# Kernel tuning notes

Measured on AMD Instinct MI355X. Metric: run time of the kernel, lower is better.

Reference implementation:

```python
import jax, jax.numpy as jnp
import numpy as np

B, N, DIM = 16, 1024, 768


def setup_inputs() -> dict:
    key = jax.random.key(0)
    ks = jax.random.split(key, 8)
    x = jax.random.normal(ks[0], (B, N, DIM), dtype=jnp.float32)
    y = jax.random.normal(ks[1], (B, N, DIM), dtype=jnp.float32)
    coords = jax.random.normal(ks[2], (N, N, 6), dtype=jnp.float32)
    # orthogonal init for U (as in torch init.orthogonal_)
    a = jax.random.normal(ks[3], (DIM, DIM), dtype=jnp.float32)
    q, r = jnp.linalg.qr(a)
    U = q * jnp.sign(jnp.diagonal(r))[None, :]
    S1 = jnp.ones((DIM,), dtype=jnp.float32)
    S2 = jnp.ones((DIM,), dtype=jnp.float32)
    gating = jnp.asarray(1.0, dtype=jnp.float32)
    temp = jnp.asarray(0.1, dtype=jnp.float32)
    pos_emb = jnp.zeros((N, 6, 1), dtype=jnp.float32)
    return {"x": x, "y": y, "coords": coords, "U": U, "S1": S1, "S2": S2,
            "gating": gating, "temp": temp, "pos_emb": pos_emb}


def reference(x, y, coords, U, S1, S2, gating, temp, pos_emb):
    dim = x.shape[-1]
    scale = dim ** (-0.5)
    # spectral decomposition: x @ U^T @ diag(S^2) @ U
    xu = x @ U.T                                   # [B,N,d]
    x1 = (xu * jnp.square(S1)) @ U                 # [B,N,d]
    x2 = (xu * jnp.square(S2)) @ U                 # [B,N,d]
    xs = jnp.stack([x1, x2], axis=1)               # [B,2,N,d]
    patch_score = jax.nn.softmax(
        jnp.einsum('bknd,bmd->bknm', xs, y) * scale, axis=-1)  # [B,2,N,M]
    pos = jnp.squeeze(coords @ pos_emb, -1)        # [N,M]
    pos_score = jax.nn.softmax(pos, axis=-1)[None, None]        # [1,1,N,M]
    g = jax.nn.sigmoid(gating)
    attn = (1.0 - g) * patch_score + g * pos_score  # [B,2,N,M]
    # entropy-routed gating
    entropy = jnp.sum(-attn * jnp.log(attn + 1e-8), axis=-1)    # [B,2,N]
    hmap = 2.0 - 2.0 * jax.nn.sigmoid(temp * jnp.transpose(entropy, (0, 2, 1)))  # [B,N,2]
    fgbg = hmap[..., 0] >= hmap[..., 1]
    route = jax.lax.stop_gradient(
        jnp.stack([fgbg, ~fgbg], axis=-1).astype(hmap.dtype))   # [B,N,2]
    heat_map = jnp.sum(hmap * route, axis=-1, keepdims=True)    # [B,N,1]
    attn_c = jnp.sum(attn * jnp.transpose(route, (0, 2, 1))[..., None], axis=1)  # [B,N,M]
    out = attn_c @ y                               # [B,N,d]
    return (out, heat_map)
```

## Files before the change

### kernel.cpp

```cpp
#include <hip/hip_runtime.h>
#include <hip/hip_bf16.h>

#define DEV __device__ __forceinline__

typedef unsigned short u16;
typedef short short8 __attribute__((ext_vector_type(8)));
typedef u16 u16x4 __attribute__((ext_vector_type(4)));
typedef float f32x16 __attribute__((ext_vector_type(16)));

static const int BB = 16;
static const int NN = 1024;
static const int DD = 768;

DEV u16 f2bf(float f) {
    unsigned u = __builtin_bit_cast(unsigned, f);
    unsigned r = u + 0x7fffu + ((u >> 16) & 1u);
    return (u16)(r >> 16);
}
DEV float h2f(u16 u) { return (float)__builtin_bit_cast(_Float16, u); }
DEV u16 f2h(float f) { return __builtin_bit_cast(u16, (_Float16)f); }

DEV void gl_lds16(const void* g, void* l) {
    __builtin_amdgcn_global_load_lds(
        (const __attribute__((address_space(1))) unsigned int*)g,
        (__attribute__((address_space(3))) unsigned int*)l, 16, 0, 0);
}

DEV void fence_bar() {
    asm volatile("" ::: "memory");
    __builtin_amdgcn_s_barrier();
    asm volatile("" ::: "memory");
}
DEV void wait_vm4() { asm volatile("s_waitcnt vmcnt(4)" ::: "memory"); }

template<int OM>
__global__ __launch_bounds__(256, 3) void gemm128(
    const u16* __restrict__ Ag, const u16* __restrict__ Bg, void* __restrict__ Cg,
    int K, int N, int zmod,
    long sA0, long sA1, long sB0, long sB1, long sC0, long sC1,
    float scale)
{
    __shared__ u16 As[128 * 64];
    __shared__ u16 Bs[128 * 64];

    int z = blockIdx.z;
    const u16* A = Ag + (long)(z % zmod) * sA0 + (long)(z / zmod) * sA1;
    const u16* B = Bg + (long)(z % zmod) * sB0 + (long)(z / zmod) * sB1;
    u16*   Cu = (u16*)Cg   + (long)(z % zmod) * sC0 + (long)(z / zmod) * sC1;
    float* Cf = (float*)Cg + (long)(z % zmod) * sC0 + (long)(z / zmod) * sC1;

    int tid  = threadIdx.x;
    int lane = tid & 63, wave = tid >> 6;
    int wm = wave & 1, wn = wave >> 1;
    int ln31 = lane & 31, khalf = lane >> 5;

    long m0 = (long)blockIdx.x * 128;
    long n0 = (long)blockIdx.y * 128;

    long aOfs[4], bOfs[4];
    u16 *lA[4], *lB[4];
#pragma unroll
    for (int i = 0; i < 4; i++) {
        int p = tid + i * 256;
        int row = p >> 3, qs = p & 7;
        int q = qs ^ (row & 7);
        aOfs[i] = (m0 + row) * (long)K + q * 8;
        bOfs[i] = (n0 + row) * (long)K + q * 8;
        lA[i] = As + p * 8;
        lB[i] = Bs + p * 8;
    }

    int aoff[2][4], boff[2][4];
#pragma unroll
    for (int t = 0; t < 2; t++) {
        int ra = wm * 64 + t * 32 + ln31;
        int rb = wn * 64 + t * 32 + ln31;
#pragma unroll
        for (int h = 0; h < 4; h++) {
            aoff[t][h] = ra * 64 + (((h * 2 + khalf) ^ (ra & 7)) * 8);
            boff[t][h] = rb * 64 + (((h * 2 + khalf) ^ (rb & 7)) * 8);
        }
    }

    f32x16 acc[2][2] = {};

    for (int k0 = 0; k0 < K; k0 += 64) {
#pragma unroll
        for (int i = 0; i < 4; i++) gl_lds16(A + aOfs[i] + k0, lA[i]);
#pragma unroll
        for (int i = 0; i < 4; i++) gl_lds16(B + bOfs[i] + k0, lB[i]);
        __syncthreads();

#pragma unroll
        for (int h = 0; h < 4; h++) {
            short8 af[2], bfr[2];
#pragma unroll
            for (int t = 0; t < 2; t++) af[t]  = *(const short8*)(As + aoff[t][h]);
#pragma unroll
            for (int t = 0; t < 2; t++) bfr[t] = *(const short8*)(Bs + boff[t][h]);
#pragma unroll
            for (int ti = 0; ti < 2; ti++)
#pragma unroll
                for (int tj = 0; tj < 2; tj++)
                    acc[ti][tj] = __builtin_amdgcn_mfma_f32_32x32x16_bf16(
                        af[ti], bfr[tj], acc[ti][tj], 0, 0, 0);
        }
        __syncthreads();
    }

    long crow = m0 + wm * 64 + 4 * khalf;
    long ccol = n0 + wn * 64 + ln31;
#pragma unroll
    for (int ti = 0; ti < 2; ti++)
#pragma unroll
        for (int tj = 0; tj < 2; tj++)
#pragma unroll
            for (int r = 0; r < 16; r++) {
                long row = crow + ti * 32 + (r & 3) + 8 * (r >> 2);
                long col = ccol + tj * 32;
                float v = acc[ti][tj][r] * scale;
                long idx = row * (long)N + col;
                if constexpr (OM == 0)      Cu[idx] = f2bf(v);
                else if constexpr (OM == 1) Cu[idx] = f2h(v);
                else                        Cf[idx] = v;
            }
}

template<int OM>
__global__ __launch_bounds__(512, 2) void gemm256(
    const u16* __restrict__ Ag, const u16* __restrict__ Bg, void* __restrict__ Cg,
    int K, int N, int zmod,
    long sA0, long sA1, long sB0, long sB1, long sC0, long sC1,
    float scale)
{
    __shared__ u16 lds[2][4][8192];

    int z = blockIdx.z;
    const u16* A = Ag + (long)(z % zmod) * sA0 + (long)(z / zmod) * sA1;
    const u16* B = Bg + (long)(z % zmod) * sB0 + (long)(z / zmod) * sB1;
    u16*   Cu = (u16*)Cg   + (long)(z % zmod) * sC0 + (long)(z / zmod) * sC1;
    float* Cf = (float*)Cg + (long)(z % zmod) * sC0 + (long)(z / zmod) * sC1;

    int tid  = threadIdx.x;
    int lane = tid & 63, wave = tid >> 6;
    int wm = wave >> 2, wn = wave & 3;
    int ln31 = lane & 31, khalf = lane >> 5;

    long m0 = (long)blockIdx.x * 256;
    long n0 = (long)blockIdx.y * 256;
    const u16* Apan = A + m0 * (long)K;
    const u16* Bpan = B + n0 * (long)K;

    long stA[2];
#pragma unroll
    for (int r = 0; r < 2; r++) {
        int p = tid + r * 512;
        int row = p >> 2, c = (p & 3) ^ ((row >> 1) & 3);
        stA[r] = (long)row * K + c * 8;
    }

    int aoffs[4][2], boffs[2][2];
#pragma unroll
    for (int m = 0; m < 4; m++) {
        int rr = wm * 128 + m * 32 + ln31;
#pragma unroll
        for (int sl = 0; sl < 2; sl++)
            aoffs[m][sl] = rr * 32 + (((sl * 2 + khalf) ^ ((rr >> 1) & 3)) * 8);
    }
#pragma unroll
    for (int n = 0; n < 2; n++) {
        int cc = wn * 64 + n * 32 + ln31;
#pragma unroll
        for (int sl = 0; sl < 2; sl++)
            boffs[n][sl] = cc * 32 + (((sl * 2 + khalf) ^ ((cc >> 1) & 3)) * 8);
    }

    f32x16 acc[4][2] = {};

    int nkt = K >> 6;
    int niter = nkt >> 1;

#define STG(PAN, BUF, HSEL, KT, KH) do {                                   \
    const u16* _s0 = (PAN) + stA[0] + (long)(KT) * 64 + (KH) * 32;         \
    const u16* _s1 = (PAN) + stA[1] + (long)(KT) * 64 + (KH) * 32;         \
    u16* _d = &lds[BUF][HSEL][0] + tid * 8;                                \
    gl_lds16(_s0, _d);                                                     \
    gl_lds16(_s1, _d + 4096);                                              \
} while (0)

#define PH(BUF, S, DOSTG, GUARD) do {                                      \
    short8 av[4], bv[2];                                                   \
    _Pragma("unroll")                                                      \
    for (int m = 0; m < 4; m++)                                            \
        av[m] = *(const short8*)(&lds[BUF][(S) >> 1][aoffs[m][(S) & 1]]);  \
    _Pragma("unroll")                                                      \
    for (int n = 0; n < 2; n++)                                            \
        bv[n] = *(const short8*)(&lds[BUF][2 + ((S) >> 1)][boffs[n][(S) & 1]]); \
    DOSTG;                                                                 \
    if (GUARD) wait_vm4();                                                 \
    fence_bar();                                                           \
    __builtin_amdgcn_s_setprio(1);                                         \
    _Pragma("unroll")                                                      \
    for (int m = 0; m < 4; m++)                                            \
        _Pragma("unroll")                                                  \
        for (int n = 0; n < 2; n++)                                        \
            acc[m][n] = __builtin_amdgcn_mfma_f32_32x32x16_bf16(           \
                av[m], bv[n], acc[m][n], 0, 0, 0);                         \
    __builtin_amdgcn_s_setprio(0);                                         \
    fence_bar();                                                           \
} while (0)

    STG(Apan, 0, 0, 0, 0);
    STG(Bpan, 0, 2, 0, 0);
    STG(Apan, 0, 1, 0, 1);
    STG(Bpan, 0, 3, 0, 1);
    STG(Apan, 1, 0, 1, 0);
    STG(Bpan, 1, 2, 1, 0);
    wait_vm4();
    fence_bar();

    for (int it = 0; it < niter; ++it) {
        int t1 = 2 * it + 1;
        int t2 = 2 * it + 2; int t2c = t2 < nkt ? t2 : nkt - 1;
        int t3 = 2 * it + 3; int t3c = t3 < nkt ? t3 : nkt - 1;
        PH(0, 0, STG(Apan, 1, 1, t1,  1), false);
        PH(0, 1, STG(Bpan, 1, 3, t1,  1), false);
        PH(0, 2, STG(Apan, 0, 0, t2c, 0), false);
        PH(0, 3, STG(Bpan, 0, 2, t2c, 0), true);
        PH(1, 0, STG(Apan, 0, 1, t2c, 1), false);
        PH(1, 1, STG(Bpan, 0, 3, t2c, 1), false);
        PH(1, 2, STG(Apan, 1, 0, t3c, 0), false);
        PH(1, 3, STG(Bpan, 1, 2, t3c, 0), true);
    }
#undef PH
#undef STG

    long crow = m0 + wm * 128 + 4 * khalf;
    long ccol = n0 + wn * 64 + ln31;
#pragma unroll
    for (int m = 0; m < 4; m++)
#pragma unroll
        for (int n = 0; n < 2; n++)
#pragma unroll
            for (int r = 0; r < 16; r++) {
                long row = crow + m * 32 + (r & 3) + 8 * (r >> 2);
                long col = ccol + n * 32;
                float v = acc[m][n][r] * scale;
                long idx = row * (long)N + col;
                if constexpr (OM == 0)      Cu[idx] = f2bf(v);
                else if constexpr (OM == 1) Cu[idx] = f2h(v);
                else                        Cf[idx] = v;
            }
}

DEV float wave_red_max(float v) {
#pragma unroll
    for (int o = 32; o; o >>= 1) v = fmaxf(v, __shfl_xor(v, o));
    return v;
}
DEV float wave_red_sum(float v) {
#pragma unroll
    for (int o = 32; o; o >>= 1) v += __shfl_xor(v, o);
    return v;
}
DEV float block_red_max(float v, float* sh) {
    v = wave_red_max(v);
    if ((threadIdx.x & 63) == 0) sh[threadIdx.x >> 6] = v;
    __syncthreads();
    v = fmaxf(fmaxf(sh[0], sh[1]), fmaxf(sh[2], sh[3]));
    __syncthreads();
    return v;
}
DEV float block_red_sum(float v, float* sh) {
    v = wave_red_sum(v);
    if ((threadIdx.x & 63) == 0) sh[threadIdx.x >> 6] = v;
    __syncthreads();
    v = (sh[0] + sh[1]) + (sh[2] + sh[3]);
    __syncthreads();
    return v;
}

__global__ __launch_bounds__(256) void k_prep_all(
    const float* __restrict__ x, const float* __restrict__ y,
    const float* __restrict__ coords, const float* __restrict__ U,
    const float* __restrict__ S1, const float* __restrict__ S2,
    const float* __restrict__ pe,
    u16* __restrict__ xb, u16* __restrict__ yb, u16* __restrict__ yT,
    u16* __restrict__ UTb, u16* __restrict__ VT1, u16* __restrict__ VT2,
    float* __restrict__ P)
{
    __shared__ float shmem[32 * 33];
    int bid = blockIdx.x, tid = threadIdx.x;

    if (bid < 12288) {
        float (*tile)[33] = (float(*)[33])shmem;
        int b = bid / 768, rem = bid % 768;
        int d0 = (rem % 24) * 32, m0 = (rem / 24) * 32;
        int r = tid >> 3, c4 = (tid & 7) * 4;
        const float* ybase = y + (long)b * NN * DD;
        float4 v = *(const float4*)(ybase + (long)(m0 + r) * DD + d0 + c4);
        u16x4 w4;
        w4[0] = f2bf(v.x); w4[1] = f2bf(v.y); w4[2] = f2bf(v.z); w4[3] = f2bf(v.w);
        *(u16x4*)(yb + (long)b * NN * DD + (long)(m0 + r) * DD + d0 + c4) = w4;
        tile[r][c4 + 0] = v.x; tile[r][c4 + 1] = v.y;
        tile[r][c4 + 2] = v.z; tile[r][c4 + 3] = v.w;
        __syncthreads();
        int d = tid >> 3, mq = (tid & 7) * 4;
        u16x4 o;
        o[0] = f2bf(tile[mq + 0][d]); o[1] = f2bf(tile[mq + 1][d]);
        o[2] = f2bf(tile[mq + 2][d]); o[3] = f2bf(tile[mq + 3][d]);
        *(u16x4*)(yT + (long)b * DD * NN + (long)(d0 + d) * NN + m0 + mq) = o;
        return;
    }
    bid -= 12288;

    if (bid < 6144) {
        long base = ((long)bid * 256 + tid) * 8;
        float4 f0 = *(const float4*)(x + base);
        float4 f1 = *(const float4*)(x + base + 4);
        short8 w;
        w[0] = (short)f2bf(f0.x); w[1] = (short)f2bf(f0.y);
        w[2] = (short)f2bf(f0.z); w[3] = (short)f2bf(f0.w);
        w[4] = (short)f2bf(f1.x); w[5] = (short)f2bf(f1.y);
        w[6] = (short)f2bf(f1.z); w[7] = (short)f2bf(f1.w);
        *(short8*)(xb + base) = w;
        return;
    }
    bid -= 6144;

    if (bid < 1024) {
        int n = bid, t = tid;
        float p6[6];
#pragma unroll
        for (int c = 0; c < 6; c++) p6[c] = pe[n * 6 + c];
        float v[4];
#pragma unroll
        for (int i = 0; i < 4; i++) {
            const float* cp = coords + ((long)n * NN + t * 4 + i) * 6;
            v[i] = p6[0]*cp[0] + p6[1]*cp[1] + p6[2]*cp[2]
                 + p6[3]*cp[3] + p6[4]*cp[4] + p6[5]*cp[5];
        }
        float mx = block_red_max(fmaxf(fmaxf(v[0], v[1]), fmaxf(v[2], v[3])), shmem);
        float e[4], s = 0.f;
#pragma unroll
        for (int i = 0; i < 4; i++) { e[i] = expf(v[i] - mx); s += e[i]; }
        float Z = block_red_sum(s, shmem);
        float inv = 1.f / Z;
        float4 o; o.x = e[0]*inv; o.y = e[1]*inv; o.z = e[2]*inv; o.w = e[3]*inv;
        *(float4*)(P + ((long)n << 10) + t * 4) = o;
        return;
    }
    bid -= 1024;

    {
        float (*tile)[33] = (float(*)[33])shmem;
        int i0 = (bid % 24) * 32, j0 = (bid / 24) * 32;
        int tx = tid & 31, ty = tid >> 5;
#pragma unroll
        for (int r = 0; r < 32; r += 8) {
            int i = i0 + ty + r, j = j0 + tx;
            tile[ty + r][tx] = U[(long)i * DD + j];
        }
        __syncthreads();
        float s1v = S1[i0 + tx];
        float s2v = S2[i0 + tx];
        s1v *= s1v; s2v *= s2v;
#pragma unroll
        for (int r = 0; r < 32; r += 8) {
            int j = j0 + ty + r, i = i0 + tx;
            float v = tile[tx][ty + r];
            UTb[(long)j * DD + i] = f2bf(v);
            VT1[(long)j * DD + i] = f2bf(s1v * v);
            VT2[(long)j * DD + i] = f2bf(s2v * v);
        }
    }
}

__global__ __launch_bounds__(64) void k_route(
    u16* __restrict__ S, const float* __restrict__ P,
    const float* __restrict__ gating, const float* __restrict__ temp,
    float* __restrict__ heat)
{
    int bn = blockIdx.x;
    int b = bn >> 10, n = bn & 1023, t = threadIdx.x;
    u16* s1p = S + ((long)(b * 2) << 20) + ((long)n << 10);
    u16* s2p = s1p + (1L << 20);
    const float* pp = P + ((long)n << 10);

    short8 r1a = *(const short8*)(s1p + t * 8);
    short8 r1b = *(const short8*)(s1p + 512 + t * 8);
    short8 r2a = *(const short8*)(s2p + t * 8);
    short8 r2b = *(const short8*)(s2p + 512 + t * 8);
    float4 pv0 = *(const float4*)(pp + t * 8);
    float4 pv1 = *(const float4*)(pp + t * 8 + 4);
    float4 pv2 = *(const float4*)(pp + 512 + t * 8);
    float4 pv3 = *(const float4*)(pp + 512 + t * 8 + 4);

    float s1[16], s2[16], p8[16];
#pragma unroll
    for (int i = 0; i < 8; i++) {
        s1[i]     = h2f((u16)r1a[i]);
        s1[i + 8] = h2f((u16)r1b[i]);
        s2[i]     = h2f((u16)r2a[i]);
        s2[i + 8] = h2f((u16)r2b[i]);
    }
    p8[0]=pv0.x;  p8[1]=pv0.y;  p8[2]=pv0.z;  p8[3]=pv0.w;
    p8[4]=pv1.x;  p8[5]=pv1.y;  p8[6]=pv1.z;  p8[7]=pv1.w;
    p8[8]=pv2.x;  p8[9]=pv2.y;  p8[10]=pv2.z; p8[11]=pv2.w;
    p8[12]=pv3.x; p8[13]=pv3.y; p8[14]=pv3.z; p8[15]=pv3.w;

    float m1 = s1[0], m2 = s2[0];
#pragma unroll
    for (int i = 1; i < 16; i++) { m1 = fmaxf(m1, s1[i]); m2 = fmaxf(m2, s2[i]); }
    float mx1 = wave_red_max(m1);
    float mx2 = wave_red_max(m2);

    float e1[16], e2[16], z1 = 0.f, z2 = 0.f;
#pragma unroll
    for (int i = 0; i < 16; i++) {
        e1[i] = expf(s1[i] - mx1); z1 += e1[i];
        e2[i] = expf(s2[i] - mx2); z2 += e2[i];
    }
    float Z1 = wave_red_sum(z1);
    float Z2 = wave_red_sum(z2);

    float g = 1.f / (1.f + expf(-gating[0]));
    float c1 = (1.f - g) / Z1, c2 = (1.f - g) / Z2;

    float a1[16], a2[16], hh1 = 0.f, hh2 = 0.f;
#pragma unroll
    for (int i = 0; i < 16; i++) {
        a1[i] = e1[i] * c1 + g * p8[i];
        a2[i] = e2[i] * c2 + g * p8[i];
        hh1 -= a1[i] * logf(a1[i] + 1e-8f);
        hh2 -= a2[i] * logf(a2[i] + 1e-8f);
    }
    float H1 = wave_red_sum(hh1);
    float H2 = wave_red_sum(hh2);

    float tv = temp[0];
    float hm0 = 2.f - 2.f / (1.f + expf(-tv * H1));
    float hm1 = 2.f - 2.f / (1.f + expf(-tv * H2));
    int ks = (hm0 >= hm1) ? 0 : 1;
    if (t == 0) heat[bn] = ks ? hm1 : hm0;

    short8 w0, w1;
#pragma unroll
    for (int i = 0; i < 8; i++) {
        w0[i] = (short)f2bf(ks ? a2[i] : a1[i]);
        w1[i] = (short)f2bf(ks ? a2[i + 8] : a1[i + 8]);
    }
    *(short8*)(s1p + t * 8) = w0;
    *(short8*)(s1p + 512 + t * 8) = w1;
}

extern "C" void kernel_launch(void* const* d_in, const int* in_sizes, int n_in,
                              void* d_out, int out_size, void* d_ws, size_t ws_size,
                              hipStream_t stream)
{
    (void)in_sizes; (void)n_in; (void)out_size; (void)ws_size;
    const float* x      = (const float*)d_in[0];
    const float* y      = (const float*)d_in[1];
    const float* coords = (const float*)d_in[2];
    const float* U      = (const float*)d_in[3];
    const float* S1     = (const float*)d_in[4];
    const float* S2     = (const float*)d_in[5];
    const float* gating = (const float*)d_in[6];
    const float* temp   = (const float*)d_in[7];
    const float* pose   = (const float*)d_in[8];

    float* out  = (float*)d_out;
    float* heat = out + (long)BB * NN * DD;

    char* w = (char*)d_ws;
    u16* UTb = (u16*)w;  w += (long)DD * DD * 2;
    u16* VT  = (u16*)w;  w += (long)2 * DD * DD * 2;
    u16* W2  = (u16*)w;  w += (long)2 * DD * DD * 2;
    u16* x12 = (u16*)w;  w += (long)2 * BB * NN * DD * 2;
    u16* yb  = (u16*)w;  w += (long)BB * NN * DD * 2;
    u16* yT  = (u16*)w;  w += (long)BB * DD * NN * 2;
    u16* S   = (u16*)w;  w += (long)BB * 2 * NN * NN * 2;
    float* P = (float*)w;

    u16* xb = S;

    const long MBN = (long)BB * NN * DD;
    const long BND = (long)NN * DD;
    const long SPL = (long)NN * NN;
    const long DSQ = (long)DD * DD;

    k_prep_all<<<dim3(20032), dim3(256), 0, stream>>>(
        x, y, coords, U, S1, S2, pose, xb, yb, yT, UTb, VT, VT + DSQ, P);

    gemm128<0><<<dim3(DD / 128, DD / 128, 2), dim3(256), 0, stream>>>(
        UTb, VT, W2, DD, DD, 2,
        0L, 0L, DSQ, 0L, DSQ, 0L, 1.0f);

    gemm256<0><<<dim3(BB * NN / 256, DD / 256, 2), dim3(512), 0, stream>>>(
        xb, W2, x12, DD, DD, 2,
        0L, 0L, DSQ, 0L, MBN, 0L, 1.0f);

    gemm256<1><<<dim3(NN / 256, NN / 256, BB * 2), dim3(512), 0, stream>>>(
        x12, yb, S, DD, NN, 2,
        MBN, BND, 0L, BND, SPL, 2 * SPL, 0.036084391824351615f);

    k_route<<<dim3(BB * NN), dim3(64), 0, stream>>>(S, P, gating, temp, heat);

    gemm256<2><<<dim3(NN / 256, DD / 256, BB), dim3(512), 0, stream>>>(
        S, yT, out, NN, DD, 1,
        0L, 2 * SPL, 0L, BND, 0L, BND, 1.0f);
}
```

Baseline: 362.5 us.

## Swizzle GEMM workgroup order, split score GEMM, pack route rows, use fast math

Adds an optional workgroup-index swizzle to the 256-tile GEMM that interleaves blocks across eight groups, meant to change which tiles run concurrently and improve cache locality. The score GEMM is split into two launches over half the batch each. The route kernel now handles two rows per 128-thread block, and several exp/log calls are replaced with the fast __expf/__logf intrinsics. The fast intrinsics trade accuracy, and the extra launch adds overhead.

Result: faster. 354.7 us (-2.2%).

```diff
diff --git a/kernel.cpp b/kernel.cpp
--- a/kernel.cpp
+++ b/kernel.cpp
@@ -131,11 +131,21 @@
     const u16* __restrict__ Ag, const u16* __restrict__ Bg, void* __restrict__ Cg,
     int K, int N, int zmod,
     long sA0, long sA1, long sB0, long sB1, long sC0, long sC1,
-    float scale)
+    float scale, int swz)
 {
     __shared__ u16 lds[2][4][8192];
 
-    int z = blockIdx.z;
+    int bx = blockIdx.x, by = blockIdx.y, bz = blockIdx.z;
+    if (swz) {
+        int gx = gridDim.x, gy = gridDim.y;
+        int nwg = gx * gy * gridDim.z;
+        int lin = bx + gx * (by + gy * bz);
+        int sw = (lin & 7) * (nwg >> 3) + (lin >> 3);
+        bx = sw % gx; int t = sw / gx;
+        by = t % gy;  bz = t / gy;
+    }
+
+    int z = bz;
     const u16* A = Ag + (long)(z % zmod) * sA0 + (long)(z / zmod) * sA1;
     const u16* B = Bg + (long)(z % zmod) * sB0 + (long)(z / zmod) * sB1;
     u16*   Cu = (u16*)Cg   + (long)(z % zmod) * sC0 + (long)(z / zmod) * sC1;
@@ -146,8 +156,8 @@
     int wm = wave >> 2, wn = wave & 3;
     int ln31 = lane & 31, khalf = lane >> 5;
 
-    long m0 = (long)blockIdx.x * 256;
-    long n0 = (long)blockIdx.y * 256;
+    long m0 = (long)bx * 256;
+    long n0 = (long)by * 256;
     const u16* Apan = A + m0 * (long)K;
     const u16* Bpan = B + n0 * (long)K;
 
@@ -343,7 +353,7 @@
         float mx = block_red_max(fmaxf(fmaxf(v[0], v[1]), fmaxf(v[2], v[3])), shmem);
         float e[4], s = 0.f;
 #pragma unroll
-        for (int i = 0; i < 4; i++) { e[i] = expf(v[i] - mx); s += e[i]; }
+        for (int i = 0; i < 4; i++) { e[i] = __expf(v[i] - mx); s += e[i]; }
         float Z = block_red_sum(s, shmem);
         float inv = 1.f / Z;
         float4 o; o.x = e[0]*inv; o.y = e[1]*inv; o.z = e[2]*inv; o.w = e[3]*inv;
@@ -376,13 +386,14 @@
     }
 }
 
-__global__ __launch_bounds__(64) void k_route(
+__global__ __launch_bounds__(128) void k_route(
     u16* __restrict__ S, const float* __restrict__ P,
     const float* __restrict__ gating, const float* __restrict__ temp,
     float* __restrict__ heat)
 {
-    int bn = blockIdx.x;
-    int b = bn >> 10, n = bn & 1023, t = threadIdx.x;
+    int bn = (blockIdx.x << 1) | (threadIdx.x >> 6);
+    int t = threadIdx.x & 63;
+    int b = bn >> 10, n = bn & 1023;
     u16* s1p = S + ((long)(b * 2) << 20) + ((long)n << 10);
     u16* s2p = s1p + (1L << 20);
     const float* pp = P + ((long)n << 10);
@@ -418,13 +429,13 @@
     float e1[16], e2[16], z1 = 0.f, z2 = 0.f;
 #pragma unroll
     for (int i = 0; i < 16; i++) {
-        e1[i] = expf(s1[i] - mx1); z1 += e1[i];
-        e2[i] = expf(s2[i] - mx2); z2 += e2[i];
+        e1[i] = __expf(s1[i] - mx1); z1 += e1[i];
+        e2[i] = __expf(s2[i] - mx2); z2 += e2[i];
     }
     float Z1 = wave_red_sum(z1);
     float Z2 = wave_red_sum(z2);
 
-    float g = 1.f / (1.f + expf(-gating[0]));
+    float g = 1.f / (1.f + __expf(-gating[0]));
     float c1 = (1.f - g) / Z1, c2 = (1.f - g) / Z2;
 
     float a1[16], a2[16], hh1 = 0.f, hh2 = 0.f;
@@ -432,15 +443,15 @@
     for (int i = 0; i < 16; i++) {
         a1[i] = e1[i] * c1 + g * p8[i];
         a2[i] = e2[i] * c2 + g * p8[i];
-        hh1 -= a1[i] * logf(a1[i] + 1e-8f);
-        hh2 -= a2[i] * logf(a2[i] + 1e-8f);
+        hh1 -= a1[i] * __logf(a1[i] + 1e-8f);
+        hh2 -= a2[i] * __logf(a2[i] + 1e-8f);
     }
     float H1 = wave_red_sum(hh1);
     float H2 = wave_red_sum(hh2);
 
     float tv = temp[0];
-    float hm0 = 2.f - 2.f / (1.f + expf(-tv * H1));
-    float hm1 = 2.f - 2.f / (1.f + expf(-tv * H2));
+    float hm0 = 2.f - 2.f / (1.f + __expf(-tv * H1));
+    float hm1 = 2.f - 2.f / (1.f + __expf(-tv * H2));
     int ks = (hm0 >= hm1) ? 0 : 1;
     if (t == 0) heat[bn] = ks ? hm1 : hm0;
 
@@ -498,15 +509,18 @@
 
     gemm256<0><<<dim3(BB * NN / 256, DD / 256, 2), dim3(512), 0, stream>>>(
         xb, W2, x12, DD, DD, 2,
-        0L, 0L, DSQ, 0L, MBN, 0L, 1.0f);
-
-    gemm256<1><<<dim3(NN / 256, NN / 256, BB * 2), dim3(512), 0, stream>>>(
+        0L, 0L, DSQ, 0L, MBN, 0L, 1.0f, 0);
+
+    gemm256<1><<<dim3(NN / 256, NN / 256, BB), dim3(512), 0, stream>>>(
         x12, yb, S, DD, NN, 2,
-        MBN, BND, 0L, BND, SPL, 2 * SPL, 0.036084391824351615f);
-
-    k_route<<<dim3(BB * NN), dim3(64), 0, stream>>>(S, P, gating, temp, heat);
+        MBN, BND, 0L, BND, SPL, 2 * SPL, 0.036084391824351615f, 1);
+    gemm256<1><<<dim3(NN / 256, NN / 256, BB), dim3(512), 0, stream>>>(
+        x12 + 8 * BND, yb + 8 * BND, S + 16 * SPL, DD, NN, 2,
+        MBN, BND, 0L, BND, SPL, 2 * SPL, 0.036084391824351615f, 1);
+
+    k_route<<<dim3(BB * NN / 2), dim3(128), 0, stream>>>(S, P, gating, temp, heat);
 
     gemm256<2><<<dim3(NN / 256, DD / 256, BB), dim3(512), 0, stream>>>(
         S, yT, out, NN, DD, 1,
-        0L, 2 * SPL, 0L, BND, 0L, BND, 1.0f);
-}
+        0L, 2 * SPL, 0L, BND, 0L, BND, 1.0f, 1);
+}
```
